# Performance work log

Measured on AMD Instinct MI355X. Metric: run time of the kernel, lower is better.

## Reference

```python
import jax, jax.numpy as jnp
import numpy as np

SIZE = 256  # output image is SIZE x SIZE


def lookup_table(size):
    # matches torch.meshgrid(indexing='ij') + stack + rot90
    lin = jnp.linspace(-1.0, 1.0, size)
    xx, yy = jnp.meshgrid(lin, lin, indexing='ij')
    t = jnp.stack([xx, yy], axis=-1)
    return jnp.rot90(t, 1, axes=(0, 1))  # [S,S,2]


def area2d(a, b, c):
    return (b[..., 0] - a[..., 0]) * (c[..., 1] - a[..., 1]) - (b[..., 1] - a[..., 1]) * (c[..., 0] - a[..., 0])


def face_normals(tris):
    n = jnp.cross(tris[:, 1] - tris[:, 0], tris[:, 2] - tris[:, 0])
    # NB: faithful to source: normalize by GLOBAL Frobenius norm (not per-face)
    return n / jnp.linalg.norm(n)


def vertex_normals(vertices, f):
    fn = face_normals(vertices[f])
    vn = jnp.zeros_like(vertices)
    vn = vn.at[f[:, 0]].add(fn).at[f[:, 1]].add(fn).at[f[:, 2]].add(fn)
    return vn / jnp.linalg.norm(vn)


def bilinear_sample(img, gx, gy):
    # torch.grid_sampler_2d, mode=bilinear, padding=zeros, align_corners=False
    # img: [C,H,W]; gx -> width axis, gy -> height axis, both in [-1,1]
    C, H, W = img.shape
    x = ((gx + 1.0) * W - 1.0) * 0.5
    y = ((gy + 1.0) * H - 1.0) * 0.5
    x0 = jnp.floor(x)
    y0 = jnp.floor(y)
    x1 = x0 + 1.0
    y1 = y0 + 1.0
    wx1 = x - x0
    wx0 = 1.0 - wx1
    wy1 = y - y0
    wy0 = 1.0 - wy1

    def gather(ix, iy):
        valid = (ix >= 0) & (ix <= W - 1) & (iy >= 0) & (iy <= H - 1)
        ixc = jnp.clip(ix, 0, W - 1).astype(jnp.int32)
        iyc = jnp.clip(iy, 0, H - 1).astype(jnp.int32)
        return img[:, iyc, ixc] * valid  # [C,...]

    return (gather(x0, y0) * (wx0 * wy0) + gather(x1, y0) * (wx1 * wy0)
            + gather(x0, y1) * (wx0 * wy1) + gather(x1, y1) * (wx1 * wy1))


def setup_inputs() -> dict:
    key = jax.random.key(0)
    k1, k2, k3, k4, k5, k6 = jax.random.split(key, 6)
    V, F, M = 1024, 256, 1024
    xy = jax.random.uniform(k1, (V, 2), minval=-1.0, maxval=1.0, dtype=jnp.float32)
    z = jax.random.uniform(k2, (V, 1), minval=0.5, maxval=1.5, dtype=jnp.float32)
    vertices = jnp.concatenate([xy, z], axis=1)
    faces = jax.random.randint(k3, (F, 3), 0, V, dtype=jnp.int64)
    uv = jax.random.uniform(k4, (M, 2), dtype=jnp.float32)
    uvfaces = jax.random.randint(k5, (F, 3), 0, M, dtype=jnp.int64)
    uvmap = jax.random.uniform(k6, (3, 256, 256), dtype=jnp.float32)
    return {"vertices": vertices, "faces": faces, "uv": uv, "uvfaces": uvfaces, "uvmap": uvmap}


def reference(vertices, faces, uv, uvfaces, uvmap):
    size = SIZE
    pts = lookup_table(size)                       # [S,S,2]
    uvn = uv * 2.0 - 1.0                            # init: uv*2-1
    tris = vertices[faces]                          # [F,3,3]
    z_inv = 1.0 / tris[:, :, 2:3]                   # [F,3,1]
    vn = vertex_normals(vertices, faces)[faces] * z_inv
    uvs = uvn[uvfaces] * z_inv
    tri9 = jnp.concatenate([tris, uvs, vn, z_inv], axis=2)  # [F,3,9]
    cullmask = face_normals(tris)[:, 2] > 0         # backface cull, eye=(0,0,1)

    t2 = tris[:, :, :2]
    A = area2d(t2[:, 0], t2[:, 1], t2[:, 2])        # [F] signed double-area
    valid_tri = cullmask & (A >= 1e-9)              # raster skips A < 1e-9
    Asafe = jnp.where(jnp.abs(A) < 1e-9, 1.0, A)

    px = pts[..., 0][None]                          # [1,S,S]
    py = pts[..., 1][None]

    def edge(a, c):
        # area2d(a, p, c) evaluated on the pixel grid: linear in p
        ax, ay = a[:, 0, None, None], a[:, 1, None, None]
        cx, cy = c[:, 0, None, None], c[:, 1, None, None]
        return (px - ax) * (cy - ay) - (py - ay) * (cx - ax)

    pAB = edge(t2[:, 1], t2[:, 0])                  # [F,S,S]
    pCB = edge(t2[:, 2], t2[:, 1])
    pCA = edge(t2[:, 0], t2[:, 2])
    cover = (pAB > 0) & (pCB > 0) & (pCA > 0) & valid_tri[:, None, None]

    w1 = pCB / Asafe[:, None, None]
    w2 = pCA / Asafe[:, None, None]
    w3 = 1.0 - w1 - w2
    zinv_p = (w1 * tri9[:, 0, 8, None, None] + w2 * tri9[:, 1, 8, None, None]
              + w3 * tri9[:, 2, 8, None, None])     # interpolated 1/z, [F,S,S]
    zinit = vertices[:, 2].min()                    # initial z-buffer value
    ptsZ = 1.0 / jnp.where(cover, zinv_p, 1.0)      # perspective-correct depth
    score = jnp.where(cover & (ptsZ >= zinit), ptsZ, -jnp.inf)
    # sequential loop with `ptsZ >= zbuffer` converges to the max-depth winner
    winner = jnp.argmax(score, axis=0)              # [S,S]
    hit = jnp.isfinite(jnp.max(score, axis=0))      # [S,S]

    take = lambda arr: jnp.take_along_axis(arr, winner[None], axis=0)[0]
    W1, W2, W3 = take(w1), take(w2), take(w3)       # [S,S]
    tri_w = tri9[winner]                            # [S,S,3,9]
    pts9 = (W1[..., None] * tri_w[..., 0, :] + W2[..., None] * tri_w[..., 1, :]
            + W3[..., None] * tri_w[..., 2, :])     # [S,S,9]
    Zw = 1.0 / jnp.where(hit, pts9[..., 8], 1.0)
    attrs = pts9[..., :8] * Zw[..., None]           # perspective-corrected attrs
    rgb = bilinear_sample(uvmap, attrs[..., 3], attrs[..., 4])  # [3,S,S]
    hitf = hit.astype(rgb.dtype)
    result = jnp.concatenate([rgb * hitf[None], hitf[None]], axis=0)  # [4,S,S]
    return result
```

## Files before the change

### kernel.cpp

```cpp
#include <hip/hip_runtime.h>
#include <math.h>

#define SIZE   256
#define NFACES 256
#define NVERTS 1024
#define NSPLIT 4

struct __align__(16) FaceData {
    float ax, ay, bx, by, cx, cy;
    float z0i, z1i, z2i;
    float u0x, u0y, u1x, u1y, u2x, u2y;
    float A;
};

__global__ __launch_bounds__(1024) void render_kernel(
    const float* __restrict__ vertices,
    const int*   __restrict__ faces,
    const float* __restrict__ uv,
    const int*   __restrict__ uvfaces,
    const float* __restrict__ uvmap,
    float* __restrict__ out)
{
#pragma clang fp contract(off)
    __shared__ FaceData fd[NFACES];
    __shared__ float sh_best[NSPLIT][256];
    __shared__ int   sh_win [NSPLIT][256];
    __shared__ float wred[16];
    __shared__ int   wcnt[4];
    __shared__ int   s_nv;

    const int t    = threadIdx.x;
    const int lane = t & 63;
    const int wv   = t >> 6;
    const int col  = t & 255;
    const int grp  = t >> 8;
    const int row  = blockIdx.x;

    const float px = (float)(-1.0 + (double)col         * (2.0/255.0));
    const float py = (float)(-1.0 + (double)(255 - row) * (2.0/255.0));

    {
        float m = vertices[3*t + 2];
        for (int off = 32; off > 0; off >>= 1)
            m = fminf(m, __shfl_down(m, off));
        if (lane == 0) wred[wv] = m;
    }

    FaceData d;
    bool keep = false;
    unsigned long long bmask = 0ull;
    int rank = 0;
    if (t < NFACES) {
        const int f  = t;
        const int i0 = faces[3*f+0], i1 = faces[3*f+1], i2 = faces[3*f+2];
        const float ax = vertices[3*i0+0], ay = vertices[3*i0+1], az = vertices[3*i0+2];
        const float bx = vertices[3*i1+0], by = vertices[3*i1+1], bz = vertices[3*i1+2];
        const float cx = vertices[3*i2+0], cy = vertices[3*i2+1], cz = vertices[3*i2+2];
        const float A = (bx-ax)*(cy-ay) - (by-ay)*(cx-ax);
        const float ymin = fminf(fminf(ay, by), cy);
        const float ymax = fmaxf(fmaxf(ay, by), cy);
        keep = (A >= 1e-9f) && (py > ymin - 1e-4f) && (py < ymax + 1e-4f);
        bmask = __ballot(keep);
        rank  = __popcll(bmask & ((1ull << lane) - 1ull));
        if (lane == 0) wcnt[wv] = (int)__popcll(bmask);
        if (keep) {
            const float z0i = 1.0f/az, z1i = 1.0f/bz, z2i = 1.0f/cz;
            const int j0 = uvfaces[3*f+0], j1 = uvfaces[3*f+1], j2 = uvfaces[3*f+2];
            d.ax = ax; d.ay = ay; d.bx = bx; d.by = by; d.cx = cx; d.cy = cy;
            d.z0i = z0i; d.z1i = z1i; d.z2i = z2i;
            d.u0x = (uv[2*j0+0]*2.0f - 1.0f) * z0i;
            d.u0y = (uv[2*j0+1]*2.0f - 1.0f) * z0i;
            d.u1x = (uv[2*j1+0]*2.0f - 1.0f) * z1i;
            d.u1y = (uv[2*j1+1]*2.0f - 1.0f) * z1i;
            d.u2x = (uv[2*j2+0]*2.0f - 1.0f) * z2i;
            d.u2y = (uv[2*j2+1]*2.0f - 1.0f) * z2i;
            d.A = A;
        }
    }
    __syncthreads();

    float zinit;
    {
        float mm = wred[0];
        #pragma unroll
        for (int i = 1; i < 16; ++i) mm = fminf(mm, wred[i]);
        zinit = mm;
    }

    if (t < NFACES) {
        int base = 0;
        #pragma unroll
        for (int w = 0; w < 4; ++w) if (w < wv) base += wcnt[w];
        if (keep) fd[base + rank] = d;
        if (t == 0) s_nv = wcnt[0] + wcnt[1] + wcnt[2] + wcnt[3];
    }
    __syncthreads();

    const int nv = s_nv;
    const int cs = (nv + NSPLIT - 1) / NSPLIT;
    int f0 = grp * cs;       if (f0 > nv) f0 = nv;
    int f1 = f0 + cs;        if (f1 > nv) f1 = nv;

    float best = -INFINITY;
    int   win  = 0;
    for (int f = f0; f < f1; ++f) {
        const FaceData &c = fd[f];
        const float pAB = (px - c.bx)*(c.ay - c.by) - (py - c.by)*(c.ax - c.bx);
        const float pCB = (px - c.cx)*(c.by - c.cy) - (py - c.cy)*(c.bx - c.cx);
        const float pCA = (px - c.ax)*(c.cy - c.ay) - (py - c.ay)*(c.cx - c.ax);
        if (pAB > 0.0f && pCB > 0.0f && pCA > 0.0f) {
            const float w1 = pCB / c.A;
            const float w2 = pCA / c.A;
            const float w3 = (1.0f - w1) - w2;
            const float zp = (w1*c.z0i + w2*c.z1i) + w3*c.z2i;
            const float z  = 1.0f / zp;
            if (z >= zinit && z > best) { best = z; win = f; }
        }
    }
    sh_best[grp][col] = best;
    sh_win [grp][col] = win;
    __syncthreads();

    if (t < 256) {
        best = -INFINITY; win = 0;
        #pragma unroll
        for (int g = 0; g < NSPLIT; ++g) {
            const float z = sh_best[g][t];
            if (z > best) { best = z; win = sh_win[g][t]; }
        }

        const bool  hit = (best > -INFINITY);
        const float hf  = hit ? 1.0f : 0.0f;
        float r0 = 0.0f, r1 = 0.0f, r2 = 0.0f;

        if (hit) {
            const FaceData &c = fd[win];
            const float pCB = (px - c.cx)*(c.by - c.cy) - (py - c.cy)*(c.bx - c.cx);
            const float pCA = (px - c.ax)*(c.cy - c.ay) - (py - c.ay)*(c.cx - c.ax);
            const float w1 = pCB / c.A;
            const float w2 = pCA / c.A;
            const float w3 = (1.0f - w1) - w2;
            const float p3 = (w1*c.u0x + w2*c.u1x) + w3*c.u2x;
            const float p4 = (w1*c.u0y + w2*c.u1y) + w3*c.u2y;
            const float p8 = (w1*c.z0i + w2*c.z1i) + w3*c.z2i;
            const float Zw = 1.0f / p8;
            const float gx = p3 * Zw;
            const float gy = p4 * Zw;

            const float x = ((gx + 1.0f)*256.0f - 1.0f)*0.5f;
            const float y = ((gy + 1.0f)*256.0f - 1.0f)*0.5f;
            const float x0f = floorf(x), y0f = floorf(y);
            const float x1f = x0f + 1.0f, y1f = y0f + 1.0f;
            const float wx1 = x - x0f, wx0 = 1.0f - wx1;
            const float wy1 = y - y0f, wy0 = 1.0f - wy1;
            const float w00 = wx0*wy0, w10 = wx1*wy0, w01 = wx0*wy1, w11 = wx1*wy1;

            {
                const bool v = (x0f >= 0.0f) && (x0f <= 255.0f) && (y0f >= 0.0f) && (y0f <= 255.0f);
                const int ix = (int)fminf(fmaxf(x0f, 0.0f), 255.0f);
                const int iy = (int)fminf(fmaxf(y0f, 0.0f), 255.0f);
                const int o  = iy*256 + ix;
                const float g0 = v ? uvmap[o]          : 0.0f;
                const float g1 = v ? uvmap[65536 + o]  : 0.0f;
                const float g2 = v ? uvmap[131072 + o] : 0.0f;
                r0 = r0 + g0*w00; r1 = r1 + g1*w00; r2 = r2 + g2*w00;
            }
            {
                const bool v = (x1f >= 0.0f) && (x1f <= 255.0f) && (y0f >= 0.0f) && (y0f <= 255.0f);
                const int ix = (int)fminf(fmaxf(x1f, 0.0f), 255.0f);
                const int iy = (int)fminf(fmaxf(y0f, 0.0f), 255.0f);
                const int o  = iy*256 + ix;
                const float g0 = v ? uvmap[o]          : 0.0f;
                const float g1 = v ? uvmap[65536 + o]  : 0.0f;
                const float g2 = v ? uvmap[131072 + o] : 0.0f;
                r0 = r0 + g0*w10; r1 = r1 + g1*w10; r2 = r2 + g2*w10;
            }
            {
                const bool v = (x0f >= 0.0f) && (x0f <= 255.0f) && (y1f >= 0.0f) && (y1f <= 255.0f);
                const int ix = (int)fminf(fmaxf(x0f, 0.0f), 255.0f);
                const int iy = (int)fminf(fmaxf(y1f, 0.0f), 255.0f);
                const int o  = iy*256 + ix;
                const float g0 = v ? uvmap[o]          : 0.0f;
                const float g1 = v ? uvmap[65536 + o]  : 0.0f;
                const float g2 = v ? uvmap[131072 + o] : 0.0f;
                r0 = r0 + g0*w01; r1 = r1 + g1*w01; r2 = r2 + g2*w01;
            }
            {
                const bool v = (x1f >= 0.0f) && (x1f <= 255.0f) && (y1f >= 0.0f) && (y1f <= 255.0f);
                const int ix = (int)fminf(fmaxf(x1f, 0.0f), 255.0f);
                const int iy = (int)fminf(fmaxf(y1f, 0.0f), 255.0f);
                const int o  = iy*256 + ix;
                const float g0 = v ? uvmap[o]          : 0.0f;
                const float g1 = v ? uvmap[65536 + o]  : 0.0f;
                const float g2 = v ? uvmap[131072 + o] : 0.0f;
                r0 = r0 + g0*w11; r1 = r1 + g1*w11; r2 = r2 + g2*w11;
            }
        }

        const int pix = row*256 + t;
        out[           pix] = r0*hf;
        out[ 65536 +   pix] = r1*hf;
        out[131072 +   pix] = r2*hf;
        out[196608 +   pix] = hf;
    }
}

extern "C" void kernel_launch(void* const* d_in, const int* in_sizes, int n_in,
                              void* d_out, int out_size, void* d_ws, size_t ws_size,
                              hipStream_t stream) {
    const float* vertices = (const float*)d_in[0];
    const int*   faces    = (const int*)  d_in[1];
    const float* uv       = (const float*)d_in[2];
    const int*   uvfaces  = (const int*)  d_in[3];
    const float* uvmap    = (const float*)d_in[4];
    float*       out      = (float*)d_out;

    render_kernel<<<SIZE, 1024, 0, stream>>>(vertices, faces, uv, uvfaces, uvmap, out);
}
```

Before: 75.31 us.

## Split rows into half-row blocks, add per-wave x-bbox culling, and float4 face layout

The grid becomes 2x256 blocks that each cover half a row, and the face list is split across 8 thread groups instead of 4. Each face now stores its x-extent, so a wave can skip faces whose x bounding box misses its 64-column span. Face data is packed into float4 records so it is read with wide shared-memory loads. Ties on equal depth are broken by the original face index so the winner stays deterministic. The per-block face setup is now done twice per row, which adds redundant work.

```diff
diff --git a/kernel.cpp b/kernel.cpp
--- a/kernel.cpp
+++ b/kernel.cpp
@@ -1,17 +1,12 @@
 #include <hip/hip_runtime.h>
 #include <math.h>
+#include <limits.h>
 
 #define SIZE   256
 #define NFACES 256
 #define NVERTS 1024
-#define NSPLIT 4
-
-struct __align__(16) FaceData {
-    float ax, ay, bx, by, cx, cy;
-    float z0i, z1i, z2i;
-    float u0x, u0y, u1x, u1y, u2x, u2y;
-    float A;
-};
+#define NSPLIT 8
+
 
 __global__ __launch_bounds__(1024) void render_kernel(
     const float* __restrict__ vertices,
@@ -22,59 +17,58 @@
     float* __restrict__ out)
 {
 #pragma clang fp contract(off)
-    __shared__ FaceData fd[NFACES];
-    __shared__ float sh_best[NSPLIT][256];
-    __shared__ int   sh_win [NSPLIT][256];
-    __shared__ float wred[16];
-    __shared__ int   wcnt[4];
-    __shared__ int   s_nv;
+    __shared__ float4 fdl[NFACES * 5];
+    __shared__ int    sfid[NFACES];
+    __shared__ float  sh_best[NSPLIT][128];
+    __shared__ int    sh_fid [NSPLIT][128];
+    __shared__ int    sh_slot[NSPLIT][128];
+    __shared__ float  wred[16];
+    __shared__ int    wcnt[4];
 
     const int t    = threadIdx.x;
     const int lane = t & 63;
     const int wv   = t >> 6;
-    const int col  = t & 255;
-    const int grp  = t >> 8;
-    const int row  = blockIdx.x;
+    const int half = blockIdx.x;
+    const int row  = blockIdx.y;
+    const int col  = (t & 127) + 128 * half;
+    const int grp  = t >> 7;
 
     const float px = (float)(-1.0 + (double)col         * (2.0/255.0));
     const float py = (float)(-1.0 + (double)(255 - row) * (2.0/255.0));
 
     {
         float m = vertices[3*t + 2];
-        for (int off = 32; off > 0; off >>= 1)
-            m = fminf(m, __shfl_down(m, off));
+        for (int off = 32; off > 0; off >>= 1) m = fminf(m, __shfl_down(m, off));
         if (lane == 0) wred[wv] = m;
     }
 
-    FaceData d;
+    float4 q0, q1, q2, q3, q4;
     bool keep = false;
-    unsigned long long bmask = 0ull;
-    int rank = 0;
+    int  rank = 0;
     if (t < NFACES) {
-        const int f  = t;
-        const int i0 = faces[3*f+0], i1 = faces[3*f+1], i2 = faces[3*f+2];
+        const int i0 = faces[3*t+0], i1 = faces[3*t+1], i2 = faces[3*t+2];
         const float ax = vertices[3*i0+0], ay = vertices[3*i0+1], az = vertices[3*i0+2];
         const float bx = vertices[3*i1+0], by = vertices[3*i1+1], bz = vertices[3*i1+2];
         const float cx = vertices[3*i2+0], cy = vertices[3*i2+1], cz = vertices[3*i2+2];
         const float A = (bx-ax)*(cy-ay) - (by-ay)*(cx-ax);
-        const float ymin = fminf(fminf(ay, by), cy);
-        const float ymax = fmaxf(fmaxf(ay, by), cy);
+        const float ymin = fminf(fminf(ay,by),cy);
+        const float ymax = fmaxf(fmaxf(ay,by),cy);
         keep = (A >= 1e-9f) && (py > ymin - 1e-4f) && (py < ymax + 1e-4f);
-        bmask = __ballot(keep);
-        rank  = __popcll(bmask & ((1ull << lane) - 1ull));
+        const unsigned long long bmask = __ballot(keep);
+        rank = __popcll(bmask & ((1ull << lane) - 1ull));
         if (lane == 0) wcnt[wv] = (int)__popcll(bmask);
         if (keep) {
             const float z0i = 1.0f/az, z1i = 1.0f/bz, z2i = 1.0f/cz;
-            const int j0 = uvfaces[3*f+0], j1 = uvfaces[3*f+1], j2 = uvfaces[3*f+2];
-            d.ax = ax; d.ay = ay; d.bx = bx; d.by = by; d.cx = cx; d.cy = cy;
-            d.z0i = z0i; d.z1i = z1i; d.z2i = z2i;
-            d.u0x = (uv[2*j0+0]*2.0f - 1.0f) * z0i;
-            d.u0y = (uv[2*j0+1]*2.0f - 1.0f) * z0i;
-            d.u1x = (uv[2*j1+0]*2.0f - 1.0f) * z1i;
-            d.u1y = (uv[2*j1+1]*2.0f - 1.0f) * z1i;
-            d.u2x = (uv[2*j2+0]*2.0f - 1.0f) * z2i;
-            d.u2y = (uv[2*j2+1]*2.0f - 1.0f) * z2i;
-            d.A = A;
+            const int j0 = uvfaces[3*t+0], j1 = uvfaces[3*t+1], j2 = uvfaces[3*t+2];
+            q0 = make_float4(ax, ay, bx, by);
+            q1 = make_float4(cx, cy, fminf(fminf(ax,bx),cx), fmaxf(fmaxf(ax,bx),cx));
+            q2 = make_float4(z0i, z1i, z2i, A);
+            q3 = make_float4((uv[2*j0+0]*2.0f - 1.0f) * z0i,
+                             (uv[2*j0+1]*2.0f - 1.0f) * z0i,
+                             (uv[2*j1+0]*2.0f - 1.0f) * z1i,
+                             (uv[2*j1+1]*2.0f - 1.0f) * z1i);
+            q4 = make_float4((uv[2*j2+0]*2.0f - 1.0f) * z2i,
+                             (uv[2*j2+1]*2.0f - 1.0f) * z2i, 0.0f, 0.0f);
         }
     }
     __syncthreads();
@@ -86,47 +80,62 @@
         for (int i = 1; i < 16; ++i) mm = fminf(mm, wred[i]);
         zinit = mm;
     }
-
-    if (t < NFACES) {
+    const int nv = wcnt[0] + wcnt[1] + wcnt[2] + wcnt[3];
+
+    if (t < NFACES && keep) {
         int base = 0;
         #pragma unroll
         for (int w = 0; w < 4; ++w) if (w < wv) base += wcnt[w];
-        if (keep) fd[base + rank] = d;
-        if (t == 0) s_nv = wcnt[0] + wcnt[1] + wcnt[2] + wcnt[3];
+        const int slot = base + rank;
+        sfid[slot] = t;
+        fdl[slot*5+0] = q0; fdl[slot*5+1] = q1; fdl[slot*5+2] = q2;
+        fdl[slot*5+3] = q3; fdl[slot*5+4] = q4;
     }
     __syncthreads();
 
-    const int nv = s_nv;
+    const int   c0   = ((t >> 6) & 1) * 64 + 128 * half;
+    const float pxlo = (float)(-1.0 + (double)c0        * (2.0/255.0));
+    const float pxhi = (float)(-1.0 + (double)(c0 + 63) * (2.0/255.0));
+
     const int cs = (nv + NSPLIT - 1) / NSPLIT;
-    int f0 = grp * cs;       if (f0 > nv) f0 = nv;
-    int f1 = f0 + cs;        if (f1 > nv) f1 = nv;
-
-    float best = -INFINITY;
-    int   win  = 0;
-    for (int f = f0; f < f1; ++f) {
-        const FaceData &c = fd[f];
-        const float pAB = (px - c.bx)*(c.ay - c.by) - (py - c.by)*(c.ax - c.bx);
-        const float pCB = (px - c.cx)*(c.by - c.cy) - (py - c.cy)*(c.bx - c.cx);
-        const float pCA = (px - c.ax)*(c.cy - c.ay) - (py - c.ay)*(c.cx - c.ax);
+    int f0 = grp * cs; if (f0 > nv) f0 = nv;
+    int f1 = f0 + cs;  if (f1 > nv) f1 = nv;
+
+    float best  = -INFINITY;
+    int   wfid  = INT_MAX;
+    int   wslot = 0;
+    for (int i = f0; i < f1; ++i) {
+        const float4 c1 = fdl[i*5+1];
+        if (c1.w + 1e-4f < pxlo || c1.z - 1e-4f > pxhi) continue;
+        const float4 c0q = fdl[i*5+0];
+        const float pAB = (px - c0q.z)*(c0q.y - c0q.w) - (py - c0q.w)*(c0q.x - c0q.z);
+        const float pCB = (px - c1.x)*(c0q.w - c1.y)   - (py - c1.y)*(c0q.z - c1.x);
+        const float pCA = (px - c0q.x)*(c1.y - c0q.y)  - (py - c0q.y)*(c1.x - c0q.x);
         if (pAB > 0.0f && pCB > 0.0f && pCA > 0.0f) {
-            const float w1 = pCB / c.A;
-            const float w2 = pCA / c.A;
+            const float4 c2 = fdl[i*5+2];
+            const float w1 = pCB / c2.w;
+            const float w2 = pCA / c2.w;
             const float w3 = (1.0f - w1) - w2;
-            const float zp = (w1*c.z0i + w2*c.z1i) + w3*c.z2i;
+            const float zp = (w1*c2.x + w2*c2.y) + w3*c2.z;
             const float z  = 1.0f / zp;
-            if (z >= zinit && z > best) { best = z; win = f; }
-        }
-    }
-    sh_best[grp][col] = best;
-    sh_win [grp][col] = win;
+            if (z >= zinit) {
+                const int fid = sfid[i];
+                if (z > best || (z == best && fid < wfid)) { best = z; wfid = fid; wslot = i; }
+            }
+        }
+    }
+    sh_best[grp][t & 127] = best;
+    sh_fid [grp][t & 127] = wfid;
+    sh_slot[grp][t & 127] = wslot;
     __syncthreads();
 
-    if (t < 256) {
-        best = -INFINITY; win = 0;
+    if (t < 128) {
+        best = -INFINITY; wfid = INT_MAX; wslot = 0;
         #pragma unroll
         for (int g = 0; g < NSPLIT; ++g) {
             const float z = sh_best[g][t];
-            if (z > best) { best = z; win = sh_win[g][t]; }
+            const int   f = sh_fid [g][t];
+            if (z > best || (z == best && f < wfid)) { best = z; wfid = f; wslot = sh_slot[g][t]; }
         }
 
         const bool  hit = (best > -INFINITY);
@@ -134,15 +143,19 @@
         float r0 = 0.0f, r1 = 0.0f, r2 = 0.0f;
 
         if (hit) {
-            const FaceData &c = fd[win];
-            const float pCB = (px - c.cx)*(c.by - c.cy) - (py - c.cy)*(c.bx - c.cx);
-            const float pCA = (px - c.ax)*(c.cy - c.ay) - (py - c.ay)*(c.cx - c.ax);
-            const float w1 = pCB / c.A;
-            const float w2 = pCA / c.A;
+            const float4 c0q = fdl[wslot*5+0];
+            const float4 c1  = fdl[wslot*5+1];
+            const float4 c2  = fdl[wslot*5+2];
+            const float4 c3  = fdl[wslot*5+3];
+            const float4 c4  = fdl[wslot*5+4];
+            const float pCB = (px - c1.x)*(c0q.w - c1.y)  - (py - c1.y)*(c0q.z - c1.x);
+            const float pCA = (px - c0q.x)*(c1.y - c0q.y) - (py - c0q.y)*(c1.x - c0q.x);
+            const float w1 = pCB / c2.w;
+            const float w2 = pCA / c2.w;
             const float w3 = (1.0f - w1) - w2;
-            const float p3 = (w1*c.u0x + w2*c.u1x) + w3*c.u2x;
-            const float p4 = (w1*c.u0y + w2*c.u1y) + w3*c.u2y;
-            const float p8 = (w1*c.z0i + w2*c.z1i) + w3*c.z2i;
+            const float p3 = (w1*c3.x + w2*c3.z) + w3*c4.x;
+            const float p4 = (w1*c3.y + w2*c3.w) + w3*c4.y;
+            const float p8 = (w1*c2.x + w2*c2.y) + w3*c2.z;
             const float Zw = 1.0f / p8;
             const float gx = p3 * Zw;
             const float gy = p4 * Zw;
@@ -197,7 +210,7 @@
             }
         }
 
-        const int pix = row*256 + t;
+        const int pix = row*256 + col;
         out[           pix] = r0*hf;
         out[ 65536 +   pix] = r1*hf;
         out[131072 +   pix] = r2*hf;
@@ -215,5 +228,6 @@
     const float* uvmap    = (const float*)d_in[4];
     float*       out      = (float*)d_out;
 
-    render_kernel<<<SIZE, 1024, 0, stream>>>(vertices, faces, uv, uvfaces, uvmap, out);
+    dim3 grid(2, SIZE);
+    render_kernel<<<grid, 1024, 0, stream>>>(vertices, faces, uv, uvfaces, uvmap, out);
 }
```

Measured after the change: 74.48 us. About the same (-1.1%).
